# Kernel tuning notes

Hardware: AMD Instinct MI355X
Metric: run time of the kernel (lower is better)

## Reference

```python
import jax, jax.numpy as jnp
import numpy as np

N = 100_000   # nodes
E = 1_600_000 # edges
IN, HID, OUT = 128, 64, 32


def _glorot(key, fan_in, fan_out):
    s = jnp.sqrt(6.0 / (fan_in + fan_out)).astype(jnp.float32)
    return jax.random.uniform(key, (fan_in, fan_out), jnp.float32, -s, s)


def setup_inputs() -> dict:
    key = jax.random.key(0)
    ks = jax.random.split(key, 8)
    x = jax.random.normal(ks[0], (N, IN), jnp.float32)
    edge_index = jax.random.randint(ks[1], (2, E), 0, N, jnp.int64)
    return {
        "x": x,
        "edge_index": edge_index,
        "W1": _glorot(ks[2], IN, HID),
        "b1": jnp.zeros((HID,), jnp.float32),
        "W_mu": _glorot(ks[3], HID, OUT),
        "b_mu": jnp.zeros((OUT,), jnp.float32),
        "W_ls": _glorot(ks[4], HID, OUT),
        "b_ls": jnp.zeros((OUT,), jnp.float32),
    }


def _gcn_conv(x, W, b, src, dst, n, dinv_sqrt):
    """PyG GCNConv: h = x @ W; symmetric-normalized scatter-add incl. self-loops; + b."""
    h = x @ W                                       # [N, F_out]
    coef = dinv_sqrt[src] * dinv_sqrt[dst]          # [E]
    msg = h[src] * coef[:, None]                    # [E, F_out] gather
    agg = jax.ops.segment_sum(msg, dst, num_segments=n)  # scatter-add
    agg = agg + h * (dinv_sqrt * dinv_sqrt)[:, None]      # self-loop contribution
    return agg + b


def reference(x, edge_index, W1, b1, W_mu, b_mu, W_ls, b_ls):
    src, dst = edge_index[0], edge_index[1]
    n = x.shape[0]
    # degree on graph with self-loops (edge weight 1), shared by all three convs
    deg = jax.ops.segment_sum(jnp.ones((src.shape[0],), x.dtype), dst, num_segments=n) + 1.0
    dinv_sqrt = jax.lax.rsqrt(deg)
    h = jax.nn.relu(_gcn_conv(x, W1, b1, src, dst, n, dinv_sqrt))
    mu = _gcn_conv(h, W_mu, b_mu, src, dst, n, dinv_sqrt)
    logstd = _gcn_conv(h, W_ls, b_ls, src, dst, n, dinv_sqrt)
    return mu, logstd
```

## Files before the change

### kernel.cpp

```cpp
#include <hip/hip_runtime.h>
#include <hip/hip_bf16.h>

#define FIN 128
#define HID 64
#define BSN 128
#define BSHIFT 7
#define SRCBITS 20
#define EPB 4096
#define BSTRIDE 2304
#define STARTBITS 21
#define SHSHIFT 14

typedef __attribute__((ext_vector_type(8))) short short8;
typedef __attribute__((ext_vector_type(4))) float floatx4;

__device__ __forceinline__ float bf2f(unsigned short u) {
    union { unsigned int i; float f; } c;
    c.i = ((unsigned int)u) << 16;
    return c.f;
}

__device__ __forceinline__ unsigned short f2bf(float f) {
    union { float f; unsigned int i; } c;
    c.f = f;
    unsigned int u = c.i;
    unsigned int r = (u + 0x7FFFu + ((u >> 16) & 1u)) >> 16;
    return (unsigned short)r;
}

__global__ void bin_fill(const int* __restrict__ src, const int* __restrict__ dst,
                         int* __restrict__ bcur, unsigned* __restrict__ rec, int E) {
    __shared__ int hist[1024];
    __shared__ int cbase[1024];
    for (int i = threadIdx.x; i < 1024; i += 256) hist[i] = 0;
    __syncthreads();
    int base = blockIdx.x * EPB;
    int lim = min(base + EPB, E);
    for (int e = base + threadIdx.x; e < lim; e += 256)
        atomicAdd(&hist[dst[e] >> BSHIFT], 1);
    __syncthreads();
    for (int b = threadIdx.x; b < 1024; b += 256) {
        int c = hist[b];
        cbase[b] = c ? atomicAdd(&bcur[b], c) : 0;
    }
    __syncthreads();
    for (int i = threadIdx.x; i < 1024; i += 256) hist[i] = 0;
    __syncthreads();
    for (int e = base + threadIdx.x; e < lim; e += 256) {
        int d = dst[e];
        int bkt = d >> BSHIFT;
        int slot = atomicAdd(&hist[bkt], 1);
        rec[bkt * BSTRIDE + cbase[bkt] + slot] =
            (unsigned)src[e] | ((unsigned)(d & (BSN - 1)) << SRCBITS);
    }
}

__global__ void csr_build(const unsigned* __restrict__ rec, const int* __restrict__ bcur,
                          unsigned* __restrict__ rowp, int* __restrict__ csr, int N) {
    __shared__ int cnt[1024], inc[1024], cur[1024];
    int b = blockIdx.x, t = threadIdx.x;
    for (int i = t; i < 1024; i += 256) { cnt[i] = 0; cur[i] = 0; }
    __syncthreads();
    int base = b * BSTRIDE;
    int cb = bcur[b];
    for (int i = t; i < cb; i += 256) {
        unsigned r = rec[base + i];
        int key = (int)((r >> SRCBITS) << 3) | (int)((r & ((1u << SRCBITS) - 1)) >> SHSHIFT);
        atomicAdd(&cnt[key], 1);
    }
    __syncthreads();
    for (int i = t; i < 1024; i += 256) inc[i] = cnt[i];
    __syncthreads();
    for (int off = 1; off < 1024; off <<= 1) {
        int tmp[4];
#pragma unroll
        for (int u = 0; u < 4; ++u) {
            int i = t + u * 256;
            tmp[u] = (i >= off) ? inc[i - off] : 0;
        }
        __syncthreads();
#pragma unroll
        for (int u = 0; u < 4; ++u) inc[t + u * 256] += tmp[u];
        __syncthreads();
    }
    if (t < BSN) {
        int kbase = t << 3;
        int s0 = (kbase == 0) ? 0 : inc[kbase - 1];
        int deg = inc[kbase + 7] - s0;
        int n = b * BSN + t;
        if (n < N)
            rowp[n] = (unsigned)(base + s0) | ((unsigned)deg << STARTBITS);
    }
    __syncthreads();
    for (int i = t; i < cb; i += 256) {
        unsigned r = rec[base + i];
        unsigned s = r & ((1u << SRCBITS) - 1);
        int key = (int)((r >> SRCBITS) << 3) | (int)(s >> SHSHIFT);
        int slot = atomicAdd(&cur[key], 1);
        csr[base + (inc[key] - cnt[key]) + slot] = (int)s;
    }
}

__global__ __launch_bounds__(256) void gemm1_mfma(
    const float* __restrict__ x, const float* __restrict__ W1,
    const unsigned* __restrict__ rowp, unsigned short* __restrict__ h0, int N) {
    __shared__ unsigned short Wt[64][136];
    {
        int t = threadIdx.x;
        int k  = t >> 1;
        int c0 = (t & 1) << 5;
        const float* wr = W1 + k * HID + c0;
#pragma unroll
        for (int cc = 0; cc < 32; ++cc)
            Wt[c0 + cc][k] = f2bf(wr[cc]);
    }
    __syncthreads();
    int wave = threadIdx.x >> 6, lane = threadIdx.x & 63;
    int m = lane & 15, q = lane >> 4;
    short8 bfr[4][4];
#pragma unroll
    for (int ct = 0; ct < 4; ++ct)
#pragma unroll
        for (int kk = 0; kk < 4; ++kk)
            bfr[ct][kk] = *((const short8*)&Wt[ct * 16 + m][kk * 32 + q * 8]);
    int ntiles = N >> 4;
    for (int t = blockIdx.x * 4 + wave; t < ntiles; t += gridDim.x * 4) {
        int nbase = t << 4;
        const float* xr = x + (size_t)(nbase + m) * FIN + q * 8;
        short8 afr[4];
#pragma unroll
        for (int kk = 0; kk < 4; ++kk) {
            float4 p0 = *((const float4*)(xr + kk * 32));
            float4 p1 = *((const float4*)(xr + kk * 32 + 4));
            short8 ta;
            ta[0] = (short)f2bf(p0.x); ta[1] = (short)f2bf(p0.y);
            ta[2] = (short)f2bf(p0.z); ta[3] = (short)f2bf(p0.w);
            ta[4] = (short)f2bf(p1.x); ta[5] = (short)f2bf(p1.y);
            ta[6] = (short)f2bf(p1.z); ta[7] = (short)f2bf(p1.w);
            afr[kk] = ta;
        }
        uint4 rp = *((const uint4*)(rowp + nbase + q * 4));
        floatx4 cacc[4];
#pragma unroll
        for (int ct = 0; ct < 4; ++ct) cacc[ct] = floatx4{0.f, 0.f, 0.f, 0.f};
#pragma unroll
        for (int ct = 0; ct < 4; ++ct)
#pragma unroll
            for (int kk = 0; kk < 4; ++kk)
                cacc[ct] = __builtin_amdgcn_mfma_f32_16x16x32_bf16(afr[kk], bfr[ct][kk], cacc[ct], 0, 0, 0);
#pragma unroll
        for (int ct = 0; ct < 4; ++ct) {
#pragma unroll
            for (int r = 0; r < 4; ++r) {
                unsigned pr = (r == 0) ? rp.x : (r == 1) ? rp.y : (r == 2) ? rp.z : rp.w;
                float d = rsqrtf((float)(pr >> STARTBITS) + 1.0f);
                int n = nbase + q * 4 + r;
                h0[(size_t)n * HID + ct * 16 + m] = f2bf(cacc[ct][r] * d);
            }
        }
    }
}


#define ACC8(a, d)                                                      \
    do {                                                                \
        union { unsigned u; float f; } c_;                              \
        c_.u = (d).x << 16;          a[0] += c_.f;                      \
        c_.u = (d).x & 0xFFFF0000u;  a[1] += c_.f;                      \
        c_.u = (d).y << 16;          a[2] += c_.f;                      \
        c_.u = (d).y & 0xFFFF0000u;  a[3] += c_.f;                      \
        c_.u = (d).z << 16;          a[4] += c_.f;                      \
        c_.u = (d).z & 0xFFFF0000u;  a[5] += c_.f;                      \
        c_.u = (d).w << 16;          a[6] += c_.f;                      \
        c_.u = (d).w & 0xFFFF0000u;  a[7] += c_.f;                      \
    } while (0)

__global__ __launch_bounds__(256, 4) void pull(
    const unsigned short* __restrict__ hp,
    const unsigned* __restrict__ rowp,
    const int* __restrict__ csr,
    const float* __restrict__ b1,
    unsigned short* __restrict__ outp,
    const float* __restrict__ Wmu, const float* __restrict__ bmu,
    const float* __restrict__ Wls, const float* __restrict__ bls,
    float* __restrict__ out, int N, int mode) {
    __shared__ unsigned short ab[32][68];
    int lane = threadIdx.x & 63;
    int wave = threadIdx.x >> 6;
    int nd8  = lane >> 3;
    int g    = lane & 7;
    int n = blockIdx.x * 32 + wave * 8 + nd8;
    bool valid = (n < N);
    int nc = valid ? n : 0;
    unsigned rp = rowp[nc];
    int start = (int)(rp & ((1u << STARTBITS) - 1u));
    int deg   = (int)(rp >> STARTBITS);
    int end   = valid ? start + deg : 0;
    if (!valid) start = 0;
    const char* hpb = (const char*)hp;
    unsigned goff = (unsigned)(g << 4);
    uint4 sv = *((const uint4*)(hpb + (((unsigned)nc) << 7) + goff));
    float di = rsqrtf((float)deg + 1.0f);
    float4 bb0 = *((const float4*)(b1 + (g << 3)));
    float4 bb1 = *((const float4*)(b1 + (g << 3) + 4));
    float a[8] = {0.f, 0.f, 0.f, 0.f, 0.f, 0.f, 0.f, 0.f};
    int j = start;
    for (; j + 8 <= end; j += 8) {
        int s0 = csr[j],     s1 = csr[j + 1], s2 = csr[j + 2], s3 = csr[j + 3];
        int s4 = csr[j + 4], s5 = csr[j + 5], s6 = csr[j + 6], s7 = csr[j + 7];
        uint4 d0 = *((const uint4*)(hpb + (((unsigned)s0) << 7) + goff));
        uint4 d1 = *((const uint4*)(hpb + (((unsigned)s1) << 7) + goff));
        uint4 d2 = *((const uint4*)(hpb + (((unsigned)s2) << 7) + goff));
        uint4 d3 = *((const uint4*)(hpb + (((unsigned)s3) << 7) + goff));
        uint4 d4 = *((const uint4*)(hpb + (((unsigned)s4) << 7) + goff));
        uint4 d5 = *((const uint4*)(hpb + (((unsigned)s5) << 7) + goff));
        uint4 d6 = *((const uint4*)(hpb + (((unsigned)s6) << 7) + goff));
        uint4 d7 = *((const uint4*)(hpb + (((unsigned)s7) << 7) + goff));
        ACC8(a, d0); ACC8(a, d1); ACC8(a, d2); ACC8(a, d3);
        ACC8(a, d4); ACC8(a, d5); ACC8(a, d6); ACC8(a, d7);
    }
    if (j + 4 <= end) {
        int s0 = csr[j], s1 = csr[j + 1], s2 = csr[j + 2], s3 = csr[j + 3];
        uint4 d0 = *((const uint4*)(hpb + (((unsigned)s0) << 7) + goff));
        uint4 d1 = *((const uint4*)(hpb + (((unsigned)s1) << 7) + goff));
        uint4 d2 = *((const uint4*)(hpb + (((unsigned)s2) << 7) + goff));
        uint4 d3 = *((const uint4*)(hpb + (((unsigned)s3) << 7) + goff));
        ACC8(a, d0); ACC8(a, d1); ACC8(a, d2); ACC8(a, d3);
        j += 4;
    }
    if (j < end) {
        int i0 = j, i1 = min(j + 1, end - 1), i2 = min(j + 2, end - 1);
        int s0 = csr[i0], s1 = csr[i1], s2 = csr[i2];
        uint4 d0 = *((const uint4*)(hpb + (((unsigned)s0) << 7) + goff));
        uint4 d1 = *((const uint4*)(hpb + (((unsigned)s1) << 7) + goff));
        uint4 d2 = *((const uint4*)(hpb + (((unsigned)s2) << 7) + goff));
        if (j + 1 >= end) { d1.x = 0u; d1.y = 0u; d1.z = 0u; d1.w = 0u; }
        if (j + 2 >= end) { d2.x = 0u; d2.y = 0u; d2.z = 0u; d2.w = 0u; }
        ACC8(a, d0); ACC8(a, d1); ACC8(a, d2);
    }
    uint4 o = {0u, 0u, 0u, 0u};
    if (valid) {
        ACC8(a, sv);
        float v[8];
        if (mode == 0) {
            float t0;
            t0 = di * a[0] + bb0.x; v[0] = (t0 > 0.f ? t0 : 0.f) * di;
            t0 = di * a[1] + bb0.y; v[1] = (t0 > 0.f ? t0 : 0.f) * di;
            t0 = di * a[2] + bb0.z; v[2] = (t0 > 0.f ? t0 : 0.f) * di;
            t0 = di * a[3] + bb0.w; v[3] = (t0 > 0.f ? t0 : 0.f) * di;
            t0 = di * a[4] + bb1.x; v[4] = (t0 > 0.f ? t0 : 0.f) * di;
            t0 = di * a[5] + bb1.y; v[5] = (t0 > 0.f ? t0 : 0.f) * di;
            t0 = di * a[6] + bb1.z; v[6] = (t0 > 0.f ? t0 : 0.f) * di;
            t0 = di * a[7] + bb1.w; v[7] = (t0 > 0.f ? t0 : 0.f) * di;
        } else {
#pragma unroll
            for (int k = 0; k < 8; ++k) v[k] = di * a[k];
        }
        o.x = (unsigned)f2bf(v[0]) | ((unsigned)f2bf(v[1]) << 16);
        o.y = (unsigned)f2bf(v[2]) | ((unsigned)f2bf(v[3]) << 16);
        o.z = (unsigned)f2bf(v[4]) | ((unsigned)f2bf(v[5]) << 16);
        o.w = (unsigned)f2bf(v[6]) | ((unsigned)f2bf(v[7]) << 16);
    }
    if (mode == 0) {
        if (valid)
            *((uint4*)(outp + (size_t)n * HID + (g << 3))) = o;
        return;
    }
    *((uint4*)&ab[wave * 8 + nd8][g << 3]) = o;
    __syncthreads();
    int m = lane & 15, q = lane >> 4;
    int tileId = wave >> 1;
    int ct0 = (wave & 1) * 2;
    short8 a0 = *((const short8*)&ab[tileId * 16 + m][q * 8]);
    short8 a1 = *((const short8*)&ab[tileId * 16 + m][32 + q * 8]);
    short8 bfr[2][2];
    float bias[2];
#pragma unroll
    for (int c = 0; c < 2; ++c) {
        int col = (ct0 + c) * 16 + m;
#pragma unroll
        for (int kk = 0; kk < 2; ++kk) {
            short8 tf;
#pragma unroll
            for (int jj = 0; jj < 8; ++jj) {
                int k = kk * 32 + q * 8 + jj;
                float w = (col < 32) ? Wmu[k * 32 + col] : Wls[k * 32 + (col - 32)];
                tf[jj] = (short)f2bf(w);
            }
            bfr[c][kk] = tf;
        }
        bias[c] = (col < 32) ? bmu[col] : bls[col - 32];
    }
    floatx4 cc[2];
#pragma unroll
    for (int c = 0; c < 2; ++c) cc[c] = floatx4{0.f, 0.f, 0.f, 0.f};
#pragma unroll
    for (int c = 0; c < 2; ++c) {
        cc[c] = __builtin_amdgcn_mfma_f32_16x16x32_bf16(a0, bfr[c][0], cc[c], 0, 0, 0);
        cc[c] = __builtin_amdgcn_mfma_f32_16x16x32_bf16(a1, bfr[c][1], cc[c], 0, 0, 0);
    }
    int nb = blockIdx.x * 32 + tileId * 16;
#pragma unroll
    for (int c = 0; c < 2; ++c) {
        int col = (ct0 + c) * 16 + m;
        int which = col >> 5, oc = col & 31;
#pragma unroll
        for (int r = 0; r < 4; ++r) {
            int n2 = nb + q * 4 + r;
            if (n2 < N)
                out[(size_t)which * N * 32 + (size_t)n2 * 32 + oc] = cc[c][r] + bias[c];
        }
    }
}

extern "C" void kernel_launch(void* const* d_in, const int* in_sizes, int n_in,
                              void* d_out, int out_size, void* d_ws, size_t ws_size,
                              hipStream_t stream) {
    const float* x   = (const float*)d_in[0];
    const int*   ei  = (const int*)d_in[1];
    const float* W1  = (const float*)d_in[2];
    const float* b1  = (const float*)d_in[3];
    const float* Wmu = (const float*)d_in[4];
    const float* bmu = (const float*)d_in[5];
    const float* Wls = (const float*)d_in[6];
    const float* bls = (const float*)d_in[7];
    int N = in_sizes[0] / FIN;
    int E = in_sizes[1] / 2;
    const int* src = ei;
    const int* dst = ei + E;
    float* out = (float*)d_out;

    int B = (N + BSN - 1) / BSN;
    int nbin = (E + EPB - 1) / EPB;

    unsigned* rowp = (unsigned*)d_ws;
    int* bcur = (int*)(rowp + N);
    int* csr  = bcur + B;
    unsigned short* bufA = (unsigned short*)(csr + (size_t)B * BSTRIDE);
    char* region2 = (char*)(bufA + (size_t)N * HID);
    unsigned* rec        = (unsigned*)region2;
    unsigned short* bufB = (unsigned short*)region2;

    hipMemsetAsync(bcur, 0, (size_t)B * sizeof(int), stream);
    bin_fill<<<nbin, 256, 0, stream>>>(src, dst, bcur, rec, E);
    csr_build<<<B, 256, 0, stream>>>(rec, bcur, rowp, csr, N);

    gemm1_mfma<<<512, 256, 0, stream>>>(x, W1, rowp, bufA, N);

    int pgrid = (N + 31) / 32;
    pull<<<pgrid, 256, 0, stream>>>(bufA, rowp, csr, b1, bufB,
                                    Wmu, bmu, Wls, bls, out, N, 0);
    pull<<<pgrid, 256, 0, stream>>>(bufB, rowp, csr, b1, (unsigned short*)0,
                                    Wmu, bmu, Wls, bls, out, N, 1);
}
```

Before: 256.4 us.

## Drop source sub-bucketing in CSR build, prefetch next indices, enlarge edge chunk

The CSR build now sorts edges by destination only. It uses a 128-entry count and scan in place of the 1024-key (dst, src-high-bits) scan, which cuts shared-memory traffic and scan barriers. It gives up the partial source ordering that may have improved gather locality in aggregation. The aggregation loop software-prefetches the next eight CSR indices before accumulating the current batch, to hide index-load latency. The bucketing kernel also processes twice as many edges per block.

```diff
diff --git a/kernel.cpp b/kernel.cpp
--- a/kernel.cpp
+++ b/kernel.cpp
@@ -6,10 +6,9 @@
 #define BSN 128
 #define BSHIFT 7
 #define SRCBITS 20
-#define EPB 4096
+#define EPB 8192
 #define BSTRIDE 2304
 #define STARTBITS 21
-#define SHSHIFT 14
 
 typedef __attribute__((ext_vector_type(8))) short short8;
 typedef __attribute__((ext_vector_type(4))) float floatx4;
@@ -57,47 +56,39 @@
 
 __global__ void csr_build(const unsigned* __restrict__ rec, const int* __restrict__ bcur,
                           unsigned* __restrict__ rowp, int* __restrict__ csr, int N) {
-    __shared__ int cnt[1024], inc[1024], cur[1024];
+    __shared__ int cnt[BSN], excl[BSN], cur[BSN];
     int b = blockIdx.x, t = threadIdx.x;
-    for (int i = t; i < 1024; i += 256) { cnt[i] = 0; cur[i] = 0; }
+    if (t < BSN) cnt[t] = 0;
     __syncthreads();
     int base = b * BSTRIDE;
     int cb = bcur[b];
+    for (int i = t; i < cb; i += 256)
+        atomicAdd(&cnt[rec[base + i] >> SRCBITS], 1);
+    __syncthreads();
+    if (t < BSN) excl[t] = cnt[t];
+    __syncthreads();
+    for (int off = 1; off < BSN; off <<= 1) {
+        int a = 0;
+        if (t < BSN && t >= off) a = excl[t - off];
+        __syncthreads();
+        if (t < BSN) excl[t] += a;
+        __syncthreads();
+    }
+    if (t < BSN) {
+        int inc = excl[t];
+        int ex = inc - cnt[t];
+        excl[t] = ex;
+        cur[t] = 0;
+        int n = b * BSN + t;
+        if (n < N)
+            rowp[n] = (unsigned)(base + ex) | ((unsigned)cnt[t] << STARTBITS);
+    }
+    __syncthreads();
     for (int i = t; i < cb; i += 256) {
         unsigned r = rec[base + i];
-        int key = (int)((r >> SRCBITS) << 3) | (int)((r & ((1u << SRCBITS) - 1)) >> SHSHIFT);
-        atomicAdd(&cnt[key], 1);
-    }
-    __syncthreads();
-    for (int i = t; i < 1024; i += 256) inc[i] = cnt[i];
-    __syncthreads();
-    for (int off = 1; off < 1024; off <<= 1) {
-        int tmp[4];
-#pragma unroll
-        for (int u = 0; u < 4; ++u) {
-            int i = t + u * 256;
-            tmp[u] = (i >= off) ? inc[i - off] : 0;
-        }
-        __syncthreads();
-#pragma unroll
-        for (int u = 0; u < 4; ++u) inc[t + u * 256] += tmp[u];
-        __syncthreads();
-    }
-    if (t < BSN) {
-        int kbase = t << 3;
-        int s0 = (kbase == 0) ? 0 : inc[kbase - 1];
-        int deg = inc[kbase + 7] - s0;
-        int n = b * BSN + t;
-        if (n < N)
-            rowp[n] = (unsigned)(base + s0) | ((unsigned)deg << STARTBITS);
-    }
-    __syncthreads();
-    for (int i = t; i < cb; i += 256) {
-        unsigned r = rec[base + i];
-        unsigned s = r & ((1u << SRCBITS) - 1);
-        int key = (int)((r >> SRCBITS) << 3) | (int)(s >> SHSHIFT);
-        int slot = atomicAdd(&cur[key], 1);
-        csr[base + (inc[key] - cnt[key]) + slot] = (int)s;
+        int dl = r >> SRCBITS;
+        int slot = atomicAdd(&cur[dl], 1);
+        csr[base + excl[dl] + slot] = (int)(r & ((1u << SRCBITS) - 1));
     }
 }
 
@@ -205,9 +196,12 @@
     float4 bb1 = *((const float4*)(b1 + (g << 3) + 4));
     float a[8] = {0.f, 0.f, 0.f, 0.f, 0.f, 0.f, 0.f, 0.f};
     int j = start;
+    int s0, s1, s2, s3, s4, s5, s6, s7;
+    if (j + 8 <= end) {
+        s0 = csr[j];     s1 = csr[j + 1]; s2 = csr[j + 2]; s3 = csr[j + 3];
+        s4 = csr[j + 4]; s5 = csr[j + 5]; s6 = csr[j + 6]; s7 = csr[j + 7];
+    }
     for (; j + 8 <= end; j += 8) {
-        int s0 = csr[j],     s1 = csr[j + 1], s2 = csr[j + 2], s3 = csr[j + 3];
-        int s4 = csr[j + 4], s5 = csr[j + 5], s6 = csr[j + 6], s7 = csr[j + 7];
         uint4 d0 = *((const uint4*)(hpb + (((unsigned)s0) << 7) + goff));
         uint4 d1 = *((const uint4*)(hpb + (((unsigned)s1) << 7) + goff));
         uint4 d2 = *((const uint4*)(hpb + (((unsigned)s2) << 7) + goff));
@@ -216,24 +210,28 @@
         uint4 d5 = *((const uint4*)(hpb + (((unsigned)s5) << 7) + goff));
         uint4 d6 = *((const uint4*)(hpb + (((unsigned)s6) << 7) + goff));
         uint4 d7 = *((const uint4*)(hpb + (((unsigned)s7) << 7) + goff));
+        if (j + 16 <= end) {
+            s0 = csr[j + 8];  s1 = csr[j + 9];  s2 = csr[j + 10]; s3 = csr[j + 11];
+            s4 = csr[j + 12]; s5 = csr[j + 13]; s6 = csr[j + 14]; s7 = csr[j + 15];
+        }
         ACC8(a, d0); ACC8(a, d1); ACC8(a, d2); ACC8(a, d3);
         ACC8(a, d4); ACC8(a, d5); ACC8(a, d6); ACC8(a, d7);
     }
     if (j + 4 <= end) {
-        int s0 = csr[j], s1 = csr[j + 1], s2 = csr[j + 2], s3 = csr[j + 3];
-        uint4 d0 = *((const uint4*)(hpb + (((unsigned)s0) << 7) + goff));
-        uint4 d1 = *((const uint4*)(hpb + (((unsigned)s1) << 7) + goff));
-        uint4 d2 = *((const uint4*)(hpb + (((unsigned)s2) << 7) + goff));
-        uint4 d3 = *((const uint4*)(hpb + (((unsigned)s3) << 7) + goff));
+        int t0 = csr[j], t1 = csr[j + 1], t2 = csr[j + 2], t3 = csr[j + 3];
+        uint4 d0 = *((const uint4*)(hpb + (((unsigned)t0) << 7) + goff));
+        uint4 d1 = *((const uint4*)(hpb + (((unsigned)t1) << 7) + goff));
+        uint4 d2 = *((const uint4*)(hpb + (((unsigned)t2) << 7) + goff));
+        uint4 d3 = *((const uint4*)(hpb + (((unsigned)t3) << 7) + goff));
         ACC8(a, d0); ACC8(a, d1); ACC8(a, d2); ACC8(a, d3);
         j += 4;
     }
     if (j < end) {
         int i0 = j, i1 = min(j + 1, end - 1), i2 = min(j + 2, end - 1);
-        int s0 = csr[i0], s1 = csr[i1], s2 = csr[i2];
-        uint4 d0 = *((const uint4*)(hpb + (((unsigned)s0) << 7) + goff));
-        uint4 d1 = *((const uint4*)(hpb + (((unsigned)s1) << 7) + goff));
-        uint4 d2 = *((const uint4*)(hpb + (((unsigned)s2) << 7) + goff));
+        int t0 = csr[i0], t1 = csr[i1], t2 = csr[i2];
+        uint4 d0 = *((const uint4*)(hpb + (((unsigned)t0) << 7) + goff));
+        uint4 d1 = *((const uint4*)(hpb + (((unsigned)t1) << 7) + goff));
+        uint4 d2 = *((const uint4*)(hpb + (((unsigned)t2) << 7) + goff));
         if (j + 1 >= end) { d1.x = 0u; d1.y = 0u; d1.z = 0u; d1.w = 0u; }
         if (j + 2 >= end) { d2.x = 0u; d2.y = 0u; d2.z = 0u; d2.w = 0u; }
         ACC8(a, d0); ACC8(a, d1); ACC8(a, d2);
```

Result: slower. 261.7 us (+2.0%).
